# Performance work log

Hardware: AMD Instinct MI355X
Metric: run time of the kernel (lower is better)

Reference implementation:

```python
import jax, jax.numpy as jnp
import numpy as np
from jax import lax

# STP parameters hard-coded in TFSTP.__init__ (stpPara)
U0 = 0.15        # u0
D_CONST = 0.05 * 20   # D = 1.0
F_CONST = 0.5 * 20    # F = 10.0
F_SMALL = 0.15        # f
R0 = 1.0


def _spike2interval(spk_bool):
    """Vectorized version of TFSTP.spike2interval.
    spk_bool: [T,H,W] bool. Returns isi [T,H,W] float32 with inf where undefined.
    For consecutive spikes s_k < s_{k+1}: isi[s_k+1 : s_{k+1}+1] = s_{k+1} - s_k.
    Equivalently isi[t] = next_spike_at_or_after(t) - last_spike_strictly_before(t).
    """
    T = spk_bool.shape[0]
    idx = jnp.arange(T, dtype=jnp.int32)[:, None, None]
    BIG = jnp.int32(T + 1)
    # last spike time <= t (running max of spike indices)
    prev_incl = lax.associative_scan(jnp.maximum, jnp.where(spk_bool, idx, -1), axis=0)
    # last spike time strictly < t (shift by one)
    prev_strict = jnp.concatenate(
        [jnp.full_like(prev_incl[:1], -1), prev_incl[:-1]], axis=0)
    # first spike time >= t (reverse running min)
    nxt = lax.associative_scan(jnp.minimum, jnp.where(spk_bool, idx, BIG),
                               axis=0, reverse=True)
    valid = (prev_strict >= 0) & (nxt < BIG)
    return jnp.where(valid, (nxt - prev_strict).astype(jnp.float32), jnp.inf)


def setup_inputs() -> dict:
    key = jax.random.key(0)
    T, H, W = 400, 250, 400
    spikes = jax.random.randint(key, (1, T, H, W), 0, 2).astype(jnp.float32)
    return {"spikes": spikes}


def reference(spikes):
    spk = spikes[0] > 0                    # [T,H,W] bool
    T, H, W = spk.shape
    half = T // 2                          # forward() breaks at t == T/2

    isi = _spike2interval(spk)             # [T,H,W]
    isi0 = isi[0]                          # prev_isi is fixed to intervals[0]

    R_init = jnp.full((H, W), R0, dtype=jnp.float32)
    u_init = jnp.full((H, W), U0, dtype=jnp.float32)

    def step(carry, xs):
        R, u = carry
        isi_t, spk_t = xs
        # update_idx = (isi_t != isi0) & (spk_t == 0) | (isi_t == 1)
        mask = ((isi_t != isi0) & (~spk_t)) | (isi_t == 1.0)
        exp_D = jnp.exp(-isi_t / D_CONST)   # exp(-inf)=0, discarded by mask
        exp_F = jnp.exp(-isi_t / F_CONST)
        R_new = jnp.where(mask, 1.0 - (1.0 - R * (1.0 - u)) * exp_D, R)
        u_new = jnp.where(mask, U0 + (u + F_SMALL * (1.0 - u) - U0) * exp_F, u)
        return (R_new, u_new), None

    # only the state at t = T//2 contributes to the output
    (R, u), _ = lax.scan(step, (R_init, u_init),
                         (isi[1:half + 1], spk[1:half + 1]))

    rho_u = -1.0 / (F_CONST * jnp.log(
        (u - U0) / (F_CONST - U0 + u * (1.0 - F_SMALL))))
    rho_R = -1.0 / (D_CONST * jnp.log(
        (1.0 - R) / (1.0 - R * (1.0 - u))))
    img = rho_u + rho_R

    mn, mx = img.min(), img.max()
    denom = jnp.where(mx == mn, 1.0, mx - mn)
    img = jnp.where(mx != mn, (img - mn) / denom, img)
    return img[None, None]  # [1,1,H,W]
```

## Files before the change

### kernel.cpp

```cpp
#include <hip/hip_runtime.h>
#include <math.h>

namespace {
constexpr int   T_STEPS = 400;
constexpr int   HALF    = 200;
constexpr int   NPIX    = 250 * 400;
constexpr int   CHUNK   = 32;
constexpr int   BLOCK   = 256;
constexpr int   NBLK    = (NPIX + BLOCK - 1) / BLOCK;
constexpr float U0      = 0.15f;
constexpr float FSMALL  = 0.15f;
}

__global__ __launch_bounds__(BLOCK) void stp_compute(
    const float* __restrict__ spikes, float* __restrict__ img,
    float* __restrict__ pmin, float* __restrict__ pmax) {
  const int  p      = blockIdx.x * BLOCK + threadIdx.x;
  const bool active = (p < NPIX);
  bool  done = !active;
  int   prev = -1;
  float R = 1.0f, u = U0;

  for (int t0 = 0; t0 < T_STEPS; t0 += CHUNK) {
    if (__syncthreads_and(done ? 1 : 0)) break;
    if (!done) {
      unsigned mask = 0u;
#pragma unroll
      for (int i = 0; i < CHUNK; ++i) {
        const float v = spikes[(size_t)(t0 + i) * NPIX + p];
        mask |= (v > 0.0f) ? (1u << i) : 0u;
      }
      while (mask) {
        const int i = __builtin_ctz(mask);
        mask &= mask - 1u;
        const int t = t0 + i;
        if (prev >= 0) {
          const int delta = t - prev;
          const int e     = (t < HALF) ? t : HALF;
          int n = e - prev;
          if (e == t && delta != 1) n -= 1;
          if (n > 0) {
            const float d  = (float)delta;
            const float eD = expf(-d);
            const float eF = expf(-(d / 10.0f));
            for (int k = 0; k < n; ++k) {
              const float Rn = 1.0f - (1.0f - R * (1.0f - u)) * eD;
              const float un = U0 + (u + FSMALL * (1.0f - u) - U0) * eF;
              R = Rn; u = un;
            }
          }
        }
        prev = t;
        if (t >= HALF) { done = true; break; }
      }
    }
  }

  float val = 0.0f;
  if (active) {
    const float lu = logf((u - U0) / (10.0f - U0 + u * (1.0f - FSMALL)));
    const float lR = logf((1.0f - R) / (1.0f - R * (1.0f - u)));
    val = (-1.0f / (10.0f * lu)) + (-1.0f / lR);
    img[p] = val;
  }

  float vmin = active ? val : INFINITY;
  float vmax = active ? val : -INFINITY;
#pragma unroll
  for (int off = 32; off > 0; off >>= 1) {
    vmin = fminf(vmin, __shfl_down(vmin, off, 64));
    vmax = fmaxf(vmax, __shfl_down(vmax, off, 64));
  }
  __shared__ float smin[BLOCK / 64], smax[BLOCK / 64];
  const int lane = threadIdx.x & 63, wid = threadIdx.x >> 6;
  if (lane == 0) { smin[wid] = vmin; smax[wid] = vmax; }
  __syncthreads();
  if (threadIdx.x == 0) {
    float mn = smin[0], mx = smax[0];
#pragma unroll
    for (int i = 1; i < BLOCK / 64; ++i) {
      mn = fminf(mn, smin[i]);
      mx = fmaxf(mx, smax[i]);
    }
    pmin[blockIdx.x] = mn;
    pmax[blockIdx.x] = mx;
  }
}

__global__ __launch_bounds__(512) void reduce_minmax(
    const float* __restrict__ pmin, const float* __restrict__ pmax,
    float* __restrict__ mm) {
  float vmin = INFINITY, vmax = -INFINITY;
  for (int i = threadIdx.x; i < NBLK; i += 512) {
    vmin = fminf(vmin, pmin[i]);
    vmax = fmaxf(vmax, pmax[i]);
  }
#pragma unroll
  for (int off = 32; off > 0; off >>= 1) {
    vmin = fminf(vmin, __shfl_down(vmin, off, 64));
    vmax = fmaxf(vmax, __shfl_down(vmax, off, 64));
  }
  __shared__ float smin[8], smax[8];
  const int lane = threadIdx.x & 63, wid = threadIdx.x >> 6;
  if (lane == 0) { smin[wid] = vmin; smax[wid] = vmax; }
  __syncthreads();
  if (threadIdx.x == 0) {
    float mn = smin[0], mx = smax[0];
#pragma unroll
    for (int i = 1; i < 8; ++i) {
      mn = fminf(mn, smin[i]);
      mx = fmaxf(mx, smax[i]);
    }
    mm[0] = mn;
    mm[1] = mx;
  }
}

__global__ __launch_bounds__(BLOCK) void normalize_k(
    float* __restrict__ img, const float* __restrict__ mm) {
  const int p = blockIdx.x * BLOCK + threadIdx.x;
  if (p < NPIX) {
    const float mn = mm[0], mx = mm[1];
    const float v  = img[p];
    img[p] = (mx != mn) ? (v - mn) / (mx - mn) : v;
  }
}

extern "C" void kernel_launch(void* const* d_in, const int* in_sizes, int n_in,
                              void* d_out, int out_size, void* d_ws, size_t ws_size,
                              hipStream_t stream) {
  const float* spikes = (const float*)d_in[0];
  float* out  = (float*)d_out;
  float* ws   = (float*)d_ws;
  float* mm   = ws;
  float* pmin = ws + 2;
  float* pmax = ws + 2 + NBLK;

  hipLaunchKernelGGL(stp_compute, dim3(NBLK), dim3(BLOCK), 0, stream,
                     spikes, out, pmin, pmax);
  hipLaunchKernelGGL(reduce_minmax, dim3(1), dim3(512), 0, stream,
                     pmin, pmax, mm);
  hipLaunchKernelGGL(normalize_k, dim3(NBLK), dim3(BLOCK), 0, stream,
                     out, mm);
}
```

Measured before the change: 79.98 us.

## Software-pipeline spike chunk loads and use single-wavefront blocks

The compute kernel is restructured so the first seven 32-step chunks are loaded into two register buffers ahead of processing, with each chunk's mask handled while the next chunk's loads are in flight. Block size drops to one wavefront, so the block-wide sync and shared-memory min/max stage are replaced by a wave vote and a direct per-wave partial write. The aim is to hide global load latency in a memory-bound scan and remove barrier stalls between divergent waves. The cost is higher register pressure from the double buffer, unconditional loads for all early chunks even for pixels that finish early, and four times more partial min/max entries for the single reduction block.

Measured after the change: 84.44 us. 1.06x slower.

```diff
diff --git a/kernel.cpp b/kernel.cpp
--- a/kernel.cpp
+++ b/kernel.cpp
@@ -6,10 +6,39 @@
 constexpr int   HALF    = 200;
 constexpr int   NPIX    = 250 * 400;
 constexpr int   CHUNK   = 32;
-constexpr int   BLOCK   = 256;
+constexpr int   BLOCK   = 64;
 constexpr int   NBLK    = (NPIX + BLOCK - 1) / BLOCK;
-constexpr float U0      = 0.15f;
-constexpr float FSMALL  = 0.15f;
+constexpr int   NORM_BLOCK = 256;
+constexpr int   NORM_NBLK  = (NPIX + NORM_BLOCK - 1) / NORM_BLOCK;
+constexpr float U0 = 0.15f;
+}
+
+__device__ __forceinline__ void apply_segment(float& R, float& u, int d, int n) {
+  const float dd = (float)d;
+  const float eD = expf(-dd);
+  const float eF = expf(-(dd / 10.0f));
+  for (int k = 0; k < n; ++k) {
+    const float Rn = 1.0f - (1.0f - R * (1.0f - u)) * eD;
+    const float un = U0 + (u + 0.15f * (1.0f - u) - U0) * eF;
+    R = Rn; u = un;
+  }
+}
+
+__device__ __forceinline__ void proc_mask(unsigned mask, int t0, int& prev,
+                                          float& R, float& u, bool& done) {
+  if (done) return;
+  while (mask) {
+    const int i = __builtin_ctz(mask);
+    mask &= mask - 1u;
+    const int t = t0 + i;
+    if (prev >= 0) {
+      const int d = t - prev;
+      const int n = (t <= HALF) ? ((d == 1) ? 1 : (d - 1)) : (HALF - prev);
+      apply_segment(R, u, d, n);
+    }
+    prev = t;
+    if (t >= HALF) { done = true; return; }
+  }
 }
 
 __global__ __launch_bounds__(BLOCK) void stp_compute(
@@ -17,48 +46,54 @@
     float* __restrict__ pmin, float* __restrict__ pmax) {
   const int  p      = blockIdx.x * BLOCK + threadIdx.x;
   const bool active = (p < NPIX);
+  const float* __restrict__ sp = spikes + (active ? p : (NPIX - 1));
+
   bool  done = !active;
   int   prev = -1;
   float R = 1.0f, u = U0;
 
-  for (int t0 = 0; t0 < T_STEPS; t0 += CHUNK) {
-    if (__syncthreads_and(done ? 1 : 0)) break;
-    if (!done) {
-      unsigned mask = 0u;
+  auto loadc = [&](float (&buf)[CHUNK], int c) {
 #pragma unroll
-      for (int i = 0; i < CHUNK; ++i) {
-        const float v = spikes[(size_t)(t0 + i) * NPIX + p];
-        mask |= (v > 0.0f) ? (1u << i) : 0u;
-      }
-      while (mask) {
-        const int i = __builtin_ctz(mask);
-        mask &= mask - 1u;
-        const int t = t0 + i;
-        if (prev >= 0) {
-          const int delta = t - prev;
-          const int e     = (t < HALF) ? t : HALF;
-          int n = e - prev;
-          if (e == t && delta != 1) n -= 1;
-          if (n > 0) {
-            const float d  = (float)delta;
-            const float eD = expf(-d);
-            const float eF = expf(-(d / 10.0f));
-            for (int k = 0; k < n; ++k) {
-              const float Rn = 1.0f - (1.0f - R * (1.0f - u)) * eD;
-              const float un = U0 + (u + FSMALL * (1.0f - u) - U0) * eF;
-              R = Rn; u = un;
-            }
-          }
-        }
-        prev = t;
-        if (t >= HALF) { done = true; break; }
-      }
+    for (int i = 0; i < CHUNK; ++i) {
+      const unsigned idx = (unsigned)(c * CHUNK + i) * (unsigned)NPIX;
+      buf[i] = sp[idx];
     }
+  };
+  auto maskof = [&](const float (&buf)[CHUNK]) -> unsigned {
+    unsigned m = 0u;
+#pragma unroll
+    for (int i = 0; i < CHUNK; ++i) m |= (buf[i] > 0.0f) ? (1u << i) : 0u;
+    return m;
+  };
+
+  float va[CHUNK], vb[CHUNK];
+  loadc(va, 0);
+  loadc(vb, 1);
+  unsigned m;
+  m = maskof(va); loadc(va, 2); proc_mask(m, 0 * CHUNK, prev, R, u, done);
+  m = maskof(vb); loadc(vb, 3); proc_mask(m, 1 * CHUNK, prev, R, u, done);
+  m = maskof(va); loadc(va, 4); proc_mask(m, 2 * CHUNK, prev, R, u, done);
+  m = maskof(vb); loadc(vb, 5); proc_mask(m, 3 * CHUNK, prev, R, u, done);
+  m = maskof(va); loadc(va, 6); proc_mask(m, 4 * CHUNK, prev, R, u, done);
+  m = maskof(vb);               proc_mask(m, 5 * CHUNK, prev, R, u, done);
+  m = maskof(va);               proc_mask(m, 6 * CHUNK, prev, R, u, done);
+
+  for (int c = 7; c <= (T_STEPS - 1) / CHUNK; ++c) {
+    if (__all((int)done)) break;
+    unsigned mt = 0u;
+#pragma unroll
+    for (int i = 0; i < CHUNK; ++i) {
+      const int t = c * CHUNK + i;
+      float v = 0.0f;
+      if (t < T_STEPS) v = sp[(unsigned)t * (unsigned)NPIX];
+      mt |= (v > 0.0f) ? (1u << i) : 0u;
+    }
+    proc_mask(mt, c * CHUNK, prev, R, u, done);
   }
 
   float val = 0.0f;
   if (active) {
-    const float lu = logf((u - U0) / (10.0f - U0 + u * (1.0f - FSMALL)));
+    const float lu = logf((u - U0) / (10.0f - U0 + u * 0.85f));
     const float lR = logf((1.0f - R) / (1.0f - R * (1.0f - u)));
     val = (-1.0f / (10.0f * lu)) + (-1.0f / lR);
     img[p] = val;
@@ -71,19 +106,9 @@
     vmin = fminf(vmin, __shfl_down(vmin, off, 64));
     vmax = fmaxf(vmax, __shfl_down(vmax, off, 64));
   }
-  __shared__ float smin[BLOCK / 64], smax[BLOCK / 64];
-  const int lane = threadIdx.x & 63, wid = threadIdx.x >> 6;
-  if (lane == 0) { smin[wid] = vmin; smax[wid] = vmax; }
-  __syncthreads();
   if (threadIdx.x == 0) {
-    float mn = smin[0], mx = smax[0];
-#pragma unroll
-    for (int i = 1; i < BLOCK / 64; ++i) {
-      mn = fminf(mn, smin[i]);
-      mx = fmaxf(mx, smax[i]);
-    }
-    pmin[blockIdx.x] = mn;
-    pmax[blockIdx.x] = mx;
+    pmin[blockIdx.x] = vmin;
+    pmax[blockIdx.x] = vmax;
   }
 }
 
@@ -116,9 +141,9 @@
   }
 }
 
-__global__ __launch_bounds__(BLOCK) void normalize_k(
+__global__ __launch_bounds__(NORM_BLOCK) void normalize_k(
     float* __restrict__ img, const float* __restrict__ mm) {
-  const int p = blockIdx.x * BLOCK + threadIdx.x;
+  const int p = blockIdx.x * NORM_BLOCK + threadIdx.x;
   if (p < NPIX) {
     const float mn = mm[0], mx = mm[1];
     const float v  = img[p];
@@ -140,6 +165,6 @@
                      spikes, out, pmin, pmax);
   hipLaunchKernelGGL(reduce_minmax, dim3(1), dim3(512), 0, stream,
                      pmin, pmax, mm);
-  hipLaunchKernelGGL(normalize_k, dim3(NBLK), dim3(BLOCK), 0, stream,
+  hipLaunchKernelGGL(normalize_k, dim3(NORM_NBLK), dim3(NORM_BLOCK), 0, stream,
                      out, mm);
 }
```
